# Kernel optimization log

Hardware: AMD Instinct MI355X
Metric: run time of the kernel (lower is better)

Reference implementation:

```python
import jax, jax.numpy as jnp
import numpy as np

TAU = 0.25
N_TIMESTEPS = 12


def setup_inputs() -> dict:
    key = jax.random.key(0)
    ks = jax.random.split(key, 6)
    B, O, H, P, C = 2048, 512, 1024, 1024, 512
    sc = lambda k, shape: jax.random.normal(k, shape, dtype=jnp.float32) * (1.0 / np.sqrt(shape[0]))
    return {
        "inputs": jax.random.normal(ks[0], (B, O), dtype=jnp.float32),
        "w_oh": sc(ks[1], (O, H)),
        "w_hp": sc(ks[2], (H, P)),
        "w_pp": sc(ks[3], (P, P)),
        "w_pc": sc(ks[4], (P, C)),
        "w_cp": sc(ks[5], (C, P)),
        "bias_h": jnp.zeros((H,), dtype=jnp.float32),
        "bias_p": jnp.zeros((P,), dtype=jnp.float32),
        "bias_c": jnp.zeros((C,), dtype=jnp.float32),
    }


def reference(inputs, w_oh, w_hp, w_pp, w_pc, w_cp, bias_h, bias_p, bias_c):
    tau = jnp.float32(TAU)
    one_m_tau = jnp.float32(1.0 - TAU)
    act = jax.nn.sigmoid
    B = inputs.shape[0]
    H, P, C = w_oh.shape[1], w_pp.shape[0], w_pc.shape[1]

    # tf.linalg.set_diag(w_pp, zeros) -> zero the self-connections
    w_pp0 = w_pp * (1.0 - jnp.eye(P, dtype=w_pp.dtype))
    # orth->hidden input is constant across timesteps
    oh = inputs @ w_oh + bias_h  # [B, H]

    h0 = jnp.zeros((B, H), dtype=inputs.dtype)
    p0 = jnp.zeros((B, P), dtype=inputs.dtype)
    c0 = jnp.zeros((B, C), dtype=inputs.dtype)
    ah0 = jnp.full((B, H), 0.5, dtype=inputs.dtype)
    ap0 = jnp.full((B, P), 0.5, dtype=inputs.dtype)
    ac0 = jnp.full((B, C), 0.5, dtype=inputs.dtype)

    def step(carry, _):
        h, p, c, ah, ap, ac = carry  # states and activations from t-1
        h_n = tau * oh + one_m_tau * h
        ah_n = act(h_n)
        # p update uses t-1 activations (per original indexing)
        p_n = tau * (ah @ w_hp + ap @ w_pp0 + ac @ w_cp + bias_p) + one_m_tau * p
        ap_n = act(p_n)
        c_n = tau * (ap @ w_pc + bias_c) + one_m_tau * c
        ac_n = act(c_n)
        return (h_n, p_n, c_n, ah_n, ap_n, ac_n), ap_n

    _, act_p_seq = jax.lax.scan(step, (h0, p0, c0, ah0, ap0, ac0), None, length=N_TIMESTEPS)
    return act_p_seq  # [T, B, P] = act_p_list[1:]
```

## Files before the change

### kernel.cpp

```cpp
#include <hip/hip_runtime.h>
#include <stdint.h>
#include <math.h>

typedef __attribute__((ext_vector_type(8))) short short8;
typedef __attribute__((ext_vector_type(4))) float floatx4;

#define B_DIM 2048
#define O_DIM 512
#define H_DIM 1024
#define P_DIM 1024
#define C_DIM 512
#define K_BIG 2560
#define K_REC 1536
#define TAU 0.25f
#define OMT 0.75f

#define VMCNT(n) (((n) & 15) | (((n) >> 4) << 14) | 0x0F70)
#define MEMFENCE asm volatile("" ::: "memory")

__device__ inline short f2bf(float f) {
  uint32_t u = __float_as_uint(f);
  u += 0x7FFFu + ((u >> 16) & 1u);
  return (short)(u >> 16);
}

__device__ inline float sigmoidf_(float x) {
  return 1.0f / (1.0f + __expf(-x));
}

__device__ inline void async_copy16(const void* g, void* l) {
  __builtin_amdgcn_global_load_lds((__attribute__((address_space(1))) void*)g,
                                   (__attribute__((address_space(3))) void*)l,
                                   16, 0, 0);
}

__device__ inline void gemm_core64(const short* __restrict__ A, int lda,
                                   const short* __restrict__ BT, int ldb,
                                   int Ktot, short* lds, floatx4 acc[2][2]) {
  const int tid = threadIdx.x, lane = tid & 63, w = tid >> 6;
  const int wm = w >> 1, wn = w & 1;
  const int fm = lane & 15, hi = lane >> 4;

  const int r0 = tid >> 3;
  const int g0 = (tid & 7) ^ (r0 & 7);
  const short* gA0 = A + (size_t)r0 * lda + g0 * 8;
  const short* gA1 = A + (size_t)(r0 + 32) * lda + g0 * 8;
  const short* gB0 = BT + (size_t)r0 * ldb + g0 * 8;
  const short* gB1 = BT + (size_t)(r0 + 32) * ldb + g0 * 8;
  const int dA0 = tid * 8, dA1 = (256 + tid) * 8;
  const int dB0 = 4096 + tid * 8, dB1 = 4096 + (256 + tid) * 8;

  const int nIter = Ktot >> 6;

  auto stage = [&](int t) {
    short* d = lds + (t % 3) * 8192;
    int ko = t * 64;
    async_copy16(gA0 + ko, d + dA0);
    async_copy16(gA1 + ko, d + dA1);
    async_copy16(gB0 + ko, d + dB0);
    async_copy16(gB1 + ko, d + dB1);
  };

  const int sw = fm & 7;

  stage(0);
  stage(1);
  for (int it = 0; it < nIter; ++it) {
    if (it + 1 < nIter) __builtin_amdgcn_s_waitcnt(VMCNT(4));
    else                __builtin_amdgcn_s_waitcnt(VMCNT(0));
    MEMFENCE;
    __builtin_amdgcn_s_barrier();
    MEMFENCE;
    if (it + 2 < nIter) stage(it + 2);
    const short* sb = lds + (it % 3) * 8192;
#pragma unroll
    for (int sl = 0; sl < 2; ++sl) {
      short8 a[2], b[2];
#pragma unroll
      for (int i = 0; i < 2; ++i) {
        int ar = wm * 32 + i * 16 + fm;
        a[i] = *(const short8*)&sb[(ar * 8 + ((sl * 4 + hi) ^ sw)) * 8];
      }
#pragma unroll
      for (int j = 0; j < 2; ++j) {
        int br = wn * 32 + j * 16 + fm;
        b[j] = *(const short8*)&sb[4096 + (br * 8 + ((sl * 4 + hi) ^ sw)) * 8];
      }
#pragma unroll
      for (int i = 0; i < 2; ++i)
#pragma unroll
        for (int j = 0; j < 2; ++j)
          acc[i][j] = __builtin_amdgcn_mfma_f32_16x16x32_bf16(a[i], b[j], acc[i][j], 0, 0, 0);
    }
  }
  MEMFENCE;
}

__device__ inline void gemm_core128(const short* __restrict__ A, int lda,
                                    const short* __restrict__ BT, int ldb,
                                    int Ktot, short* lds, floatx4 acc[4][2]) {
  const int tid = threadIdx.x, lane = tid & 63, w = tid >> 6;
  const int wm = w >> 1, wn = w & 1;
  const int fm = lane & 15, hi = lane >> 4;

  const int r0 = tid >> 3;
  const int g0 = (tid & 7) ^ (r0 & 7);
  const short* gA0 = A + (size_t)r0 * lda + g0 * 8;
  const short* gA1 = A + (size_t)(r0 + 32) * lda + g0 * 8;
  const short* gA2 = A + (size_t)(r0 + 64) * lda + g0 * 8;
  const short* gA3 = A + (size_t)(r0 + 96) * lda + g0 * 8;
  const short* gB0 = BT + (size_t)r0 * ldb + g0 * 8;
  const short* gB1 = BT + (size_t)(r0 + 32) * ldb + g0 * 8;
  const int dA0 = tid * 8,          dA1 = (256 + tid) * 8;
  const int dA2 = (512 + tid) * 8,  dA3 = (768 + tid) * 8;
  const int dB0 = 8192 + tid * 8,   dB1 = 8192 + (256 + tid) * 8;

  const int nIter = Ktot >> 6;

  auto stage = [&](int t) {
    short* d = lds + (t % 3) * 12288;
    int ko = t * 64;
    async_copy16(gA0 + ko, d + dA0);
    async_copy16(gA1 + ko, d + dA1);
    async_copy16(gA2 + ko, d + dA2);
    async_copy16(gA3 + ko, d + dA3);
    async_copy16(gB0 + ko, d + dB0);
    async_copy16(gB1 + ko, d + dB1);
  };

  const int sw = fm & 7;

  stage(0);
  stage(1);
  for (int it = 0; it < nIter; ++it) {
    if (it + 1 < nIter) __builtin_amdgcn_s_waitcnt(VMCNT(6));
    else                __builtin_amdgcn_s_waitcnt(VMCNT(0));
    MEMFENCE;
    __builtin_amdgcn_s_barrier();
    MEMFENCE;
    if (it + 2 < nIter) stage(it + 2);
    const short* sb = lds + (it % 3) * 12288;
#pragma unroll
    for (int sl = 0; sl < 2; ++sl) {
      short8 a[4], b[2];
#pragma unroll
      for (int i = 0; i < 4; ++i) {
        int ar = wm * 64 + i * 16 + fm;
        a[i] = *(const short8*)&sb[(ar * 8 + ((sl * 4 + hi) ^ sw)) * 8];
      }
#pragma unroll
      for (int j = 0; j < 2; ++j) {
        int br = wn * 32 + j * 16 + fm;
        b[j] = *(const short8*)&sb[8192 + (br * 8 + ((sl * 4 + hi) ^ sw)) * 8];
      }
#pragma unroll
      for (int i = 0; i < 4; ++i)
#pragma unroll
        for (int j = 0; j < 2; ++j)
          acc[i][j] = __builtin_amdgcn_mfma_f32_16x16x32_bf16(a[i], b[j], acc[i][j], 0, 0, 0);
    }
  }
  MEMFENCE;
}

__device__ inline void gemm_core256x128(const short* __restrict__ A, int lda,
                                        const short* __restrict__ BT, int ldb,
                                        int Ktot, short* lds, floatx4 acc[4][4]) {
  const int tid = threadIdx.x, lane = tid & 63, w = tid >> 6;
  const int wm = w >> 1, wn = w & 1;
  const int fm = lane & 15, hi = lane >> 4;

  const int r0 = tid >> 2;
  const int c0 = tid & 3;
  const int g0 = c0 ^ ((r0 >> 1) & 3);
  const short* gA0 = A + (size_t)r0 * lda + g0 * 8;
  const short* gA1 = A + (size_t)(r0 + 128) * lda + g0 * 8;
  const short* gB0 = BT + (size_t)r0 * ldb + g0 * 8;
  const int dA0 = tid * 8, dA1 = (512 + tid) * 8;
  const int dB0 = 8192 + tid * 8;

  const int nIter = Ktot >> 5;

  auto stage = [&](int t) {
    short* d = lds + (t % 3) * 12288;
    int ko = t * 32;
    async_copy16(gA0 + ko, d + dA0);
    async_copy16(gA1 + ko, d + dA1);
    async_copy16(gB0 + ko, d + dB0);
  };

  const int swz = (fm >> 1) & 3;

  stage(0);
  stage(1);
  for (int it = 0; it < nIter; ++it) {
    if (it + 1 < nIter) __builtin_amdgcn_s_waitcnt(VMCNT(3));
    else                __builtin_amdgcn_s_waitcnt(VMCNT(0));
    MEMFENCE;
    __builtin_amdgcn_s_barrier();
    MEMFENCE;
    if (it + 2 < nIter) stage(it + 2);
    const short* sb = lds + (it % 3) * 12288;
    short8 a[4], b[4];
#pragma unroll
    for (int i = 0; i < 4; ++i) {
      int ar = wm * 64 + i * 16 + fm;
      a[i] = *(const short8*)&sb[(ar * 4 + (hi ^ swz)) * 8];
    }
#pragma unroll
    for (int j = 0; j < 4; ++j) {
      int br = wn * 64 + j * 16 + fm;
      b[j] = *(const short8*)&sb[8192 + (br * 4 + (hi ^ swz)) * 8];
    }
#pragma unroll
    for (int i = 0; i < 4; ++i)
#pragma unroll
      for (int j = 0; j < 4; ++j)
        acc[i][j] = __builtin_amdgcn_mfma_f32_16x16x32_bf16(a[i], b[j], acc[i][j], 0, 0, 0);
  }
  MEMFENCE;
}


__global__ void k_build_all(const float* __restrict__ w_hp, const float* __restrict__ w_pp,
                            const float* __restrict__ w_cp, const float* __restrict__ w_pc,
                            const float* __restrict__ w_oh, const float* __restrict__ inp,
                            short* __restrict__ WbT, short* __restrict__ WpcT,
                            short* __restrict__ WohT, short* __restrict__ inb) {
  int bx = blockIdx.x, tid = threadIdx.x;
  if (bx < 10240) {
    int idx = bx * 256 + tid;
    int n = idx / K_BIG, k = idx - n * K_BIG;
    float v;
    if (k < 1024) v = w_hp[k * P_DIM + n];
    else if (k < 2048) { int r = k - 1024; v = (r == n) ? 0.f : w_pp[r * P_DIM + n]; }
    else v = w_cp[(k - 2048) * P_DIM + n];
    WbT[idx] = f2bf(v);
  } else if (bx < 12288) {
    int idx = (bx - 10240) * 256 + tid;
    int n = idx >> 10, k = idx & 1023;
    WpcT[idx] = f2bf(w_pc[k * C_DIM + n]);
  } else if (bx < 14336) {
    int idx = (bx - 12288) * 256 + tid;
    int n = idx >> 9, k = idx & 511;
    WohT[idx] = f2bf(w_oh[k * H_DIM + n]);
  } else {
    int idx = (bx - 14336) * 256 + tid;
    inb[idx] = f2bf(inp[idx]);
  }
}

__global__ __launch_bounds__(256, 2) void k_gemm_oh_ah(const short* __restrict__ inb,
                                                       const short* __restrict__ WohT,
                                                       const float* __restrict__ bias_h,
                                                       short* __restrict__ Ah) {
  __shared__ short lds[36864];
  floatx4 acc[4][2] = {};
  int m0 = (blockIdx.x & 15) * 128, n0 = (blockIdx.x >> 4) * 64;
  gemm_core128(inb + (size_t)m0 * O_DIM, O_DIM, WohT + (size_t)n0 * O_DIM, O_DIM,
               O_DIM, lds, acc);
  const int lane = threadIdx.x & 63;
  const int fm = lane & 15, hi = lane >> 4;
  const int w = threadIdx.x >> 6, wm = w >> 1, wn = w & 1;
#pragma unroll
  for (int i = 0; i < 4; ++i)
#pragma unroll
    for (int j = 0; j < 2; ++j)
#pragma unroll
      for (int r = 0; r < 4; ++r) {
        int n = n0 + wn * 32 + j * 16 + fm;
        acc[i][j][r] += bias_h[n];
      }
  float o = 1.0f;
  for (int tp = 1; tp <= 11; ++tp) {
    o *= OMT;
    float ct = 1.0f - o;
    short* dst = Ah + (size_t)(tp - 1) * B_DIM * H_DIM;
#pragma unroll
    for (int i = 0; i < 4; ++i)
#pragma unroll
      for (int j = 0; j < 2; ++j)
#pragma unroll
        for (int r = 0; r < 4; ++r) {
          int m = m0 + wm * 64 + i * 16 + hi * 4 + r;
          int n = n0 + wn * 32 + j * 16 + fm;
          dst[(size_t)m * H_DIM + n] = f2bf(sigmoidf_(ct * acc[i][j][r]));
        }
  }
}

__global__ __launch_bounds__(512, 4) void k_pah(const short* __restrict__ Ah,
                                                const short* __restrict__ WbT,
                                                float* __restrict__ Pdst) {
  __shared__ short lds[36864];
  floatx4 acc[4][4] = {};
  int logical = (blockIdx.x & 7) * 88 + (blockIdx.x >> 3);
  int m = logical >> 3, n = logical & 7;
  int m0 = m * 256, n0 = n * 128;
  gemm_core256x128(Ah + (size_t)m0 * H_DIM, H_DIM, WbT + (size_t)n0 * K_BIG, K_BIG,
                   H_DIM, lds, acc);
  const int lane = threadIdx.x & 63;
  const int fm = lane & 15, hi = lane >> 4;
  const int w = threadIdx.x >> 6, wm = w >> 1, wn = w & 1;
#pragma unroll
  for (int i = 0; i < 4; ++i)
#pragma unroll
    for (int j = 0; j < 4; ++j)
#pragma unroll
      for (int r = 0; r < 4; ++r) {
        int rr = m0 + wm * 64 + i * 16 + hi * 4 + r;
        int nn = n0 + wn * 64 + j * 16 + fm;
        Pdst[(size_t)rr * P_DIM + nn] = acc[i][j][r];
      }
}

__global__ void k_step1a(const short* __restrict__ WbT, const short* __restrict__ WpcT,
                         const float* __restrict__ bias_p, const float* __restrict__ bias_c,
                         float* __restrict__ p1v, float* __restrict__ ap1v,
                         float* __restrict__ c1v, float* __restrict__ ac1v) {
  int r = blockIdx.x * 4 + (threadIdx.x >> 6);
  int lane = threadIdx.x & 63;
  float s = 0.f;
  if (r < 1024) {
    const short* row = WbT + (size_t)r * K_BIG;
    for (int k = lane; k < K_BIG; k += 64)
      s += __uint_as_float(((uint32_t)(uint16_t)row[k]) << 16);
  } else {
    const short* row = WpcT + (size_t)(r - 1024) * P_DIM;
    for (int k = lane; k < P_DIM; k += 64)
      s += __uint_as_float(((uint32_t)(uint16_t)row[k]) << 16);
  }
#pragma unroll
  for (int off = 32; off > 0; off >>= 1) s += __shfl_down(s, off, 64);
  if (lane == 0) {
    if (r < 1024) {
      float pv = TAU * (0.5f * s + bias_p[r]);
      p1v[r] = pv; ap1v[r] = sigmoidf_(pv);
    } else {
      int n = r - 1024;
      float cv = TAU * (0.5f * s + bias_c[n]);
      c1v[n] = cv; ac1v[n] = sigmoidf_(cv);
    }
  }
}

__global__ void k_step1b(const float* __restrict__ p1v, const float* __restrict__ ap1v,
                         const float* __restrict__ c1v, const float* __restrict__ ac1v,
                         short* __restrict__ X1, float* __restrict__ p,
                         float* __restrict__ c, float* __restrict__ out0) {
  int n = blockIdx.x * 256 + threadIdx.x;
  int m = blockIdx.y;
  if (n < 1024) {
    float ap = ap1v[n];
    X1[(size_t)m * K_REC + n] = f2bf(ap);
    out0[(size_t)m * P_DIM + n] = ap;
    p[(size_t)m * P_DIM + n] = p1v[n];
  } else {
    int nn = n - 1024;
    X1[(size_t)m * K_REC + n] = f2bf(ac1v[nn]);
    c[(size_t)m * C_DIM + nn] = c1v[nn];
  }
}

__global__ __launch_bounds__(256, 3) void k_step(const short* __restrict__ Xc,
                                                 short* __restrict__ Xn,
                                                 const short* __restrict__ WbT,
                                                 const short* __restrict__ WpcT,
                                                 const float* __restrict__ bias_p,
                                                 const float* __restrict__ bias_c,
                                                 float* __restrict__ p,
                                                 float* __restrict__ c,
                                                 float* __restrict__ out_t) {
  __shared__ short lds[24576];
  floatx4 acc[2][2] = {};
  const int lane = threadIdx.x & 63;
  const int fm = lane & 15, hi = lane >> 4;
  const int w = threadIdx.x >> 6, wm = w >> 1, wn = w & 1;
  const int bx = blockIdx.x;

  if (bx < 512) {
    int m0 = (bx & 31) * 64, n0 = (bx >> 5) * 64;
    gemm_core64(Xc + (size_t)m0 * K_REC, K_REC,
                WbT + (size_t)n0 * K_BIG + H_DIM, K_BIG,
                K_REC, lds, acc);
#pragma unroll
    for (int i = 0; i < 2; ++i)
#pragma unroll
      for (int j = 0; j < 2; ++j)
#pragma unroll
        for (int r = 0; r < 4; ++r) {
          int m = m0 + wm * 32 + i * 16 + hi * 4 + r;
          int n = n0 + wn * 32 + j * 16 + fm;
          size_t o = (size_t)m * P_DIM + n;
          float pn = TAU * (acc[i][j][r] + out_t[o] + bias_p[n]) + OMT * p[o];
          p[o] = pn;
          float ap = sigmoidf_(pn);
          out_t[o] = ap;
          Xn[(size_t)m * K_REC + n] = f2bf(ap);
        }
  } else {
    int v = bx - 512;
    int m0 = (v >> 3) * 64, n0 = (v & 7) * 64;
    gemm_core64(Xc + (size_t)m0 * K_REC, K_REC,
                WpcT + (size_t)n0 * P_DIM, P_DIM,
                P_DIM, lds, acc);
#pragma unroll
    for (int i = 0; i < 2; ++i)
#pragma unroll
      for (int j = 0; j < 2; ++j)
#pragma unroll
        for (int r = 0; r < 4; ++r) {
          int m = m0 + wm * 32 + i * 16 + hi * 4 + r;
          int n = n0 + wn * 32 + j * 16 + fm;
          size_t o = (size_t)m * C_DIM + n;
          float cn = TAU * (acc[i][j][r] + bias_c[n]) + OMT * c[o];
          c[o] = cn;
          Xn[(size_t)m * K_REC + H_DIM + n] = f2bf(sigmoidf_(cn));
        }
  }
}

extern "C" void kernel_launch(void* const* d_in, const int* in_sizes, int n_in,
                              void* d_out, int out_size, void* d_ws, size_t ws_size,
                              hipStream_t stream) {
  const float* inputs = (const float*)d_in[0];
  const float* w_oh   = (const float*)d_in[1];
  const float* w_hp   = (const float*)d_in[2];
  const float* w_pp   = (const float*)d_in[3];
  const float* w_pc   = (const float*)d_in[4];
  const float* w_cp   = (const float*)d_in[5];
  const float* bias_h = (const float*)d_in[6];
  const float* bias_p = (const float*)d_in[7];
  const float* bias_c = (const float*)d_in[8];
  float* out = (float*)d_out;

  char* ws = (char*)d_ws;
  auto alloc = [&](size_t bytes) {
    char* q = ws;
    ws += (bytes + 255) & ~(size_t)255;
    return q;
  };
  short* WbT  = (short*)alloc((size_t)P_DIM * K_BIG * 2);
  short* WpcT = (short*)alloc((size_t)C_DIM * P_DIM * 2);
  short* WohT = (short*)alloc((size_t)H_DIM * O_DIM * 2);
  short* inb  = (short*)alloc((size_t)B_DIM * O_DIM * 2);
  short* Ah   = (short*)alloc((size_t)11 * B_DIM * H_DIM * 2);
  short* XA   = (short*)alloc((size_t)B_DIM * K_REC * 2);
  short* XB   = (short*)alloc((size_t)B_DIM * K_REC * 2);
  float* p    = (float*)alloc((size_t)B_DIM * P_DIM * 4);
  float* c    = (float*)alloc((size_t)B_DIM * C_DIM * 4);
  float* p1v  = (float*)alloc(1024 * 4);
  float* ap1v = (float*)alloc(1024 * 4);
  float* c1v  = (float*)alloc(512 * 4);
  float* ac1v = (float*)alloc(512 * 4);

  k_build_all<<<dim3(18432), 256, 0, stream>>>(w_hp, w_pp, w_cp, w_pc, w_oh, inputs,
                                               WbT, WpcT, WohT, inb);

  k_gemm_oh_ah<<<dim3(256), 256, 0, stream>>>(inb, WohT, bias_h, Ah);

  k_pah<<<dim3(704), 512, 0, stream>>>(Ah, WbT, out + (size_t)B_DIM * P_DIM);

  k_step1a<<<dim3(384), 256, 0, stream>>>(WbT, WpcT, bias_p, bias_c, p1v, ap1v, c1v, ac1v);
  k_step1b<<<dim3(6, 2048), 256, 0, stream>>>(p1v, ap1v, c1v, ac1v, XA, p, c, out);

  short* Xs[2] = {XB, XA};
  for (int t = 2; t <= 12; ++t) {
    k_step<<<dim3(768), 256, 0, stream>>>(Xs[(t - 1) & 1], Xs[t & 1],
                                          WbT, WpcT, bias_p, bias_c, p, c,
                                          out + (size_t)(t - 1) * B_DIM * P_DIM);
  }
}
```

Baseline: 463.1 us.

## Collapse timestep two into per-column vector math, skipping one recurrent GEMM step

Because the step-1 state is identical for every batch row, the recurrent and c-path contributions at step 2 reduce to vector-matrix products computed once, in k_qvec. A cheap elementwise kernel, k_step2, then combines them with the precomputed hidden-path term, so one full k_step GEMM launch is no longer needed. The c-path tiles are also remapped so that neighbouring blocks share a weight column tile, which should improve cache reuse. The risk is small numeric differences from the bf16 rounding inside the vector reduction, and the added small kernel launches.

```diff
diff --git a/kernel.cpp b/kernel.cpp
--- a/kernel.cpp
+++ b/kernel.cpp
@@ -23,6 +23,12 @@
   u += 0x7FFFu + ((u >> 16) & 1u);
   return (short)(u >> 16);
 }
+
+__device__ inline float bf2f(short s) {
+  return __uint_as_float(((uint32_t)(uint16_t)s) << 16);
+}
+
+__device__ inline float bfround(float f) { return bf2f(f2bf(f)); }
 
 __device__ inline float sigmoidf_(float x) {
   return 1.0f / (1.0f + __expf(-x));
@@ -323,12 +329,10 @@
   float s = 0.f;
   if (r < 1024) {
     const short* row = WbT + (size_t)r * K_BIG;
-    for (int k = lane; k < K_BIG; k += 64)
-      s += __uint_as_float(((uint32_t)(uint16_t)row[k]) << 16);
+    for (int k = lane; k < K_BIG; k += 64) s += bf2f(row[k]);
   } else {
     const short* row = WpcT + (size_t)(r - 1024) * P_DIM;
-    for (int k = lane; k < P_DIM; k += 64)
-      s += __uint_as_float(((uint32_t)(uint16_t)row[k]) << 16);
+    for (int k = lane; k < P_DIM; k += 64) s += bf2f(row[k]);
   }
 #pragma unroll
   for (int off = 32; off > 0; off >>= 1) s += __shfl_down(s, off, 64);
@@ -344,21 +348,63 @@
   }
 }
 
-__global__ void k_step1b(const float* __restrict__ p1v, const float* __restrict__ ap1v,
-                         const float* __restrict__ c1v, const float* __restrict__ ac1v,
-                         short* __restrict__ X1, float* __restrict__ p,
-                         float* __restrict__ c, float* __restrict__ out0) {
+__global__ void k_qvec(const short* __restrict__ WbT, const short* __restrict__ WpcT,
+                       const float* __restrict__ bias_p, const float* __restrict__ bias_c,
+                       const float* __restrict__ p1v, const float* __restrict__ ap1v,
+                       const float* __restrict__ c1v, const float* __restrict__ ac1v,
+                       float* __restrict__ Q, float* __restrict__ C2,
+                       short* __restrict__ ac2b) {
+  int r = blockIdx.x * 4 + (threadIdx.x >> 6);
+  int lane = threadIdx.x & 63;
+  float s = 0.f;
+  if (r < 1024) {
+    const short* row = WbT + (size_t)r * K_BIG + H_DIM;
+    for (int k = lane; k < K_REC; k += 64) {
+      float xv = (k < P_DIM) ? bfround(ap1v[k]) : bfround(ac1v[k - P_DIM]);
+      s += xv * bf2f(row[k]);
+    }
+  } else {
+    int nn = r - 1024;
+    const short* row = WpcT + (size_t)nn * P_DIM;
+    for (int k = lane; k < P_DIM; k += 64)
+      s += bfround(ap1v[k]) * bf2f(row[k]);
+  }
+#pragma unroll
+  for (int off = 32; off > 0; off >>= 1) s += __shfl_down(s, off, 64);
+  if (lane == 0) {
+    if (r < 1024) {
+      Q[r] = TAU * (s + bias_p[r]) + OMT * p1v[r];
+    } else {
+      int nn = r - 1024;
+      float cv = TAU * (s + bias_c[nn]) + OMT * c1v[nn];
+      C2[nn] = cv;
+      ac2b[nn] = f2bf(sigmoidf_(cv));
+    }
+  }
+}
+
+__global__ void k_out0(const float* __restrict__ ap1v, float* __restrict__ out0) {
+  int n = blockIdx.x * 256 + threadIdx.x;
+  out0[(size_t)blockIdx.y * P_DIM + n] = ap1v[n];
+}
+
+__global__ void k_step2(const float* __restrict__ Q, const float* __restrict__ C2,
+                        const short* __restrict__ ac2b, float* __restrict__ p,
+                        float* __restrict__ c, float* __restrict__ out1,
+                        short* __restrict__ X2) {
   int n = blockIdx.x * 256 + threadIdx.x;
   int m = blockIdx.y;
-  if (n < 1024) {
-    float ap = ap1v[n];
-    X1[(size_t)m * K_REC + n] = f2bf(ap);
-    out0[(size_t)m * P_DIM + n] = ap;
-    p[(size_t)m * P_DIM + n] = p1v[n];
+  if (n < P_DIM) {
+    size_t o = (size_t)m * P_DIM + n;
+    float pn = TAU * out1[o] + Q[n];
+    p[o] = pn;
+    float ap = sigmoidf_(pn);
+    out1[o] = ap;
+    X2[(size_t)m * K_REC + n] = f2bf(ap);
   } else {
-    int nn = n - 1024;
-    X1[(size_t)m * K_REC + n] = f2bf(ac1v[nn]);
-    c[(size_t)m * C_DIM + nn] = c1v[nn];
+    int nn = n - P_DIM;
+    X2[(size_t)m * K_REC + n] = ac2b[nn];
+    c[(size_t)m * C_DIM + nn] = C2[nn];
   }
 }
 
@@ -400,7 +446,8 @@
         }
   } else {
     int v = bx - 512;
-    int m0 = (v >> 3) * 64, n0 = (v & 7) * 64;
+    int idx = v >> 3;
+    int m0 = ((v & 7) + 8 * (idx & 3)) * 64, n0 = (idx >> 2) * 64;
     gemm_core64(Xc + (size_t)m0 * K_REC, K_REC,
                 WpcT + (size_t)n0 * P_DIM, P_DIM,
                 P_DIM, lds, acc);
@@ -453,6 +500,9 @@
   float* ap1v = (float*)alloc(1024 * 4);
   float* c1v  = (float*)alloc(512 * 4);
   float* ac1v = (float*)alloc(512 * 4);
+  float* Qv   = (float*)alloc(1024 * 4);
+  float* C2v  = (float*)alloc(512 * 4);
+  short* ac2b = (short*)alloc(512 * 2);
 
   k_build_all<<<dim3(18432), 256, 0, stream>>>(w_hp, w_pp, w_cp, w_pc, w_oh, inputs,
                                                WbT, WpcT, WohT, inb);
@@ -462,10 +512,14 @@
   k_pah<<<dim3(704), 512, 0, stream>>>(Ah, WbT, out + (size_t)B_DIM * P_DIM);
 
   k_step1a<<<dim3(384), 256, 0, stream>>>(WbT, WpcT, bias_p, bias_c, p1v, ap1v, c1v, ac1v);
-  k_step1b<<<dim3(6, 2048), 256, 0, stream>>>(p1v, ap1v, c1v, ac1v, XA, p, c, out);
+  k_qvec<<<dim3(384), 256, 0, stream>>>(WbT, WpcT, bias_p, bias_c,
+                                        p1v, ap1v, c1v, ac1v, Qv, C2v, ac2b);
+  k_out0<<<dim3(4, 2048), 256, 0, stream>>>(ap1v, out);
+  k_step2<<<dim3(6, 2048), 256, 0, stream>>>(Qv, C2v, ac2b, p, c,
+                                             out + (size_t)B_DIM * P_DIM, XB);
 
   short* Xs[2] = {XB, XA};
-  for (int t = 2; t <= 12; ++t) {
+  for (int t = 3; t <= 12; ++t) {
     k_step<<<dim3(768), 256, 0, stream>>>(Xs[(t - 1) & 1], Xs[t & 1],
                                           WbT, WpcT, bias_p, bias_c, p, c,
                                           out + (size_t)(t - 1) * B_DIM * P_DIM);
```

After: 448.4 us. -3.2%, faster.
